# Kernel optimization log

Hardware: AMD Instinct MI355X
Metric: run time of the kernel (lower is better)

Reference implementation:

```python
import jax, jax.numpy as jnp
import numpy as np

N = 100000
E = 1600000
IN, HID, OUT = 128, 256, 128


def setup_inputs() -> dict:
    key = jax.random.key(0)
    ks = jax.random.split(key, 8)
    x = jax.random.normal(ks[0], (N, IN), dtype=jnp.float32)
    edge_index = jax.random.randint(ks[1], (2, E), 0, N, dtype=jnp.int64)
    # PyG SAGEConv params: lin_l (neighbor aggr, with bias), lin_r (root, no bias)
    def glorot(k, shape):
        fan_in = shape[1]
        return jax.random.normal(k, shape, dtype=jnp.float32) / jnp.sqrt(jnp.float32(fan_in))
    W1l = glorot(ks[2], (HID, IN)); b1 = jnp.zeros((HID,), jnp.float32)
    W1r = glorot(ks[3], (HID, IN))
    W2l = glorot(ks[4], (OUT, HID)); b2 = jnp.zeros((OUT,), jnp.float32)
    W2r = glorot(ks[5], (OUT, HID))
    return {"x": x, "edge_index": edge_index, "W1l": W1l, "b1": b1,
            "W1r": W1r, "W2l": W2l, "b2": b2, "W2r": W2r}


def sage_conv(x, row, col, Wl, b, Wr, n_nodes):
    # mean-aggregate neighbor features x[row] at target nodes col
    msg = x[row]                                               # [E, d]
    s = jax.ops.segment_sum(msg, col, num_segments=n_nodes)    # [N, d]
    deg = jax.ops.segment_sum(jnp.ones((row.shape[0], 1), x.dtype), col,
                              num_segments=n_nodes)            # [N, 1]
    mean = s / jnp.maximum(deg, 1.0)
    return mean @ Wl.T + b + x @ Wr.T


def reference(x, edge_index, W1l, b1, W1r, W2l, b2, W2r):
    row, col = edge_index[0], edge_index[1]
    h = sage_conv(x, row, col, W1l, b1, W1r, N)
    h = jax.nn.relu(h)
    # dropout is identity in eval mode
    out = sage_conv(h, row, col, W2l, b2, W2r, N)
    return out
```

## Files before the change

### kernel.cpp

```cpp
#include <hip/hip_runtime.h>
#include <hip/hip_bf16.h>
#include <hip/hip_fp16.h>

#define NN 100000
#define NE 1600000
#define NCHUNK ((NN + 127) / 128)
#define NPB 512
#define NB 256
#define CHUNK 8192
#define NCH ((NE + CHUNK - 1) / CHUNK)

typedef __attribute__((ext_vector_type(8))) short short8;
typedef __attribute__((ext_vector_type(4))) float float4v;
typedef __attribute__((ext_vector_type(2))) float float2v;

__device__ __forceinline__ unsigned short f2bf(float f) {
    unsigned int b = __float_as_uint(f);
    return (unsigned short)((b + 0x7fffu + ((b >> 16) & 1u)) >> 16);
}
__device__ __forceinline__ unsigned int pack_bf16(float lo, float hi) {
    return (unsigned int)f2bf(lo) | ((unsigned int)f2bf(hi) << 16);
}
__device__ __forceinline__ void addp8(float* a, uint2 u) {
    float2v f;
    f = __builtin_amdgcn_cvt_pk_f32_fp8(u.x, false); a[0] += f.x; a[1] += f.y;
    f = __builtin_amdgcn_cvt_pk_f32_fp8(u.x, true);  a[2] += f.x; a[3] += f.y;
    f = __builtin_amdgcn_cvt_pk_f32_fp8(u.y, false); a[4] += f.x; a[5] += f.y;
    f = __builtin_amdgcn_cvt_pk_f32_fp8(u.y, true);  a[6] += f.x; a[7] += f.y;
}
__device__ __forceinline__ unsigned char f2fp8(float v) {
    int r = __builtin_amdgcn_cvt_pk_fp8_f32(v, v, 0, false);
    return (unsigned char)(r & 0xff);
}
__device__ __forceinline__ unsigned short pack2fp8(float lo, float hi) {
    int r = __builtin_amdgcn_cvt_pk_fp8_f32(lo, hi, 0, false);
    return (unsigned short)(r & 0xffff);
}
__device__ __forceinline__ float h2f(unsigned short u) {
    return __half2float(__ushort_as_half(u));
}

__global__ void k_prep(const float* x, const float* W1l, const float* W1r,
                       const float* W2l, const float* W2r, const int* ei,
                       unsigned int* axb_u, unsigned short* xf8, unsigned short* wb1,
                       unsigned short* wb2, int* bcnt) {
    __shared__ int hh[NB];
    int b = blockIdx.x, t = threadIdx.x;
    if (b < 25000) {
        int tt = b * 256 + t;
        int node = tt >> 6, i = tt & 63;
        float2 v = ((const float2*)x)[tt];
        axb_u[(size_t)node * 128 + 64 + i] = pack_bf16(v.x, v.y);
        xf8[(size_t)node * 64 + i] = pack2fp8(v.x, v.y);
    } else if (b < 25128) {
        int i = (b - 25000) * 256 + t;
        int r1 = i >> 7, c1 = i & 127;
        wb1[r1 * 256 + c1]       = f2bf(W1l[i]);
        wb1[r1 * 256 + 128 + c1] = f2bf(W1r[i]);
        wb2[i]         = f2bf(W2l[i]);
        wb2[32768 + i] = f2bf(W2r[i]);
    } else {
        hh[t] = 0;
        __syncthreads();
        int e0 = (b - 25128) * 6250;
        for (int e = e0 + t; e < e0 + 6250; e += 256)
            atomicAdd(&hh[ei[NE + e] >> 9], 1);
        __syncthreads();
        if (hh[t]) atomicAdd(&bcnt[t], hh[t]);
    }
}

__global__ void k_bscan(const int* bcnt, int* boff, int* bcur) {
    __shared__ int s[NB];
    int t = threadIdx.x;
    int v = bcnt[t];
    s[t] = v;
    __syncthreads();
    for (int d = 1; d < NB; d <<= 1) {
        int val = (t >= d) ? s[t - d] : 0;
        __syncthreads();
        s[t] += val;
        __syncthreads();
    }
    boff[t + 1] = s[t];
    if (t == 0) boff[0] = 0;
    bcur[t] = s[t] - v;
}

__global__ __launch_bounds__(256) void k_bscatter(const int* ei, int* bcur, unsigned int* pairs) {
    __shared__ unsigned int buf[CHUNK];
    __shared__ int cnt[NB];
    __shared__ int lbase[NB];
    __shared__ int lcur[NB];
    __shared__ int gpos[NB];
    int t = threadIdx.x;
    int e0 = blockIdx.x * CHUNK;
    int nedge = NE - e0; if (nedge > CHUNK) nedge = CHUNK;
    cnt[t] = 0;
    __syncthreads();
    for (int i = t; i < nedge; i += 256)
        atomicAdd(&cnt[ei[NE + e0 + i] >> 9], 1);
    __syncthreads();
    int v = cnt[t];
    lcur[t] = v;
    __syncthreads();
    for (int d = 1; d < NB; d <<= 1) {
        int val = (t >= d) ? lcur[t - d] : 0;
        __syncthreads();
        lcur[t] += val;
        __syncthreads();
    }
    lbase[t] = lcur[t] - v;
    gpos[t] = atomicAdd(&bcur[t], v);
    __syncthreads();
    lcur[t] = lbase[t];
    __syncthreads();
    for (int i = t; i < nedge; i += 256) {
        int r = ei[e0 + i], c = ei[NE + e0 + i];
        int b = c >> 9;
        int p = atomicAdd(&lcur[b], 1);
        buf[p] = (unsigned)r | ((unsigned)(c & 511) << 17);
    }
    __syncthreads();
    int wv = t >> 6, lane = t & 63;
    for (int b = wv; b < NB; b += 4) {
        int n = cnt[b], lb = lbase[b], gp = gpos[b];
        for (int i = lane; i < n; i += 64)
            pairs[gp + i] = buf[lb + i];
    }
}

__global__ __launch_bounds__(256) void k_build(const unsigned int* pairs, const int* boff,
                                               int* off, int* deg, int* csr) {
    __shared__ int ldeg[NPB];
    __shared__ int lcur[NPB];
    __shared__ int sscan[256];
    int b = blockIdx.x;
    int nbase = b * NPB;
    if (nbase >= NN) return;
    int t = threadIdx.x;
    int base = boff[b], cntb = boff[b + 1] - base;
    ldeg[t] = 0; ldeg[t + 256] = 0;
    __syncthreads();
    for (int i = t; i < cntb; i += 256) {
        unsigned int pr = pairs[base + i];
        atomicAdd(&ldeg[pr >> 17], 1);
    }
    __syncthreads();
    int d0 = ldeg[2 * t], d1 = ldeg[2 * t + 1];
    int v = d0 + d1;
    sscan[t] = v;
    __syncthreads();
    for (int d = 1; d < 256; d <<= 1) {
        int val = (t >= d) ? sscan[t - d] : 0;
        __syncthreads();
        sscan[t] += val;
        __syncthreads();
    }
    int ex = sscan[t] - v;
    lcur[2 * t] = ex; lcur[2 * t + 1] = ex + d0;
    __syncthreads();
    int nloc = NN - nbase; if (nloc > NPB) nloc = NPB;
    for (int ln = t; ln < nloc; ln += 256) {
        off[nbase + ln] = base + lcur[ln];
        deg[nbase + ln] = ldeg[ln];
    }
    __syncthreads();
    for (int i = t; i < cntb; i += 256) {
        unsigned int pr = pairs[base + i];
        int p = atomicAdd(&lcur[pr >> 17], 1);
        csr[base + p] = (int)(pr & 0x1FFFFu);
    }
}

__global__ void k_agg1(const uint2* xf8, const int* off, const int* deg,
                       const int* csr, unsigned int* axb_w) {
    int wid = (blockIdx.x * 256 + threadIdx.x) >> 6;
    if (wid >= NN) return;
    int lane = threadIdx.x & 63;
    int sub = lane >> 4, l16 = lane & 15;
    int start = off[wid], d = deg[wid];
    const uint2* gp = xf8 + l16;
    float a[8] = {0.f, 0.f, 0.f, 0.f, 0.f, 0.f, 0.f, 0.f};
    int j = sub;
    for (; j + 4 < d; j += 8) {
        int n0 = csr[start + j];
        int n1 = csr[start + j + 4];
        uint2 u0 = gp[(size_t)n0 * 16];
        uint2 u1 = gp[(size_t)n1 * 16];
        addp8(a, u0); addp8(a, u1);
    }
    if (j < d) {
        int nb = csr[start + j];
        uint2 u = gp[(size_t)nb * 16];
        addp8(a, u);
    }
#pragma unroll
    for (int i = 0; i < 8; i++) {
        a[i] += __shfl_xor(a[i], 16, 64);
        a[i] += __shfl_xor(a[i], 32, 64);
    }
    if (sub == 0) {
        float inv = 1.0f / (float)(d > 0 ? d : 1);
        uint4 o;
        o.x = pack_bf16(a[0] * inv, a[1] * inv);
        o.y = pack_bf16(a[2] * inv, a[3] * inv);
        o.z = pack_bf16(a[4] * inv, a[5] * inv);
        o.w = pack_bf16(a[6] * inv, a[7] * inv);
        *(uint4*)(axb_w + (size_t)wid * 128 + (l16 << 2)) = o;
    }
}

__global__ void k_agg2(const uint2* g, const int* off, const int* deg,
                       const int* csr, const unsigned short* partial, float* out) {
    int wid = (blockIdx.x * 256 + threadIdx.x) >> 6;
    if (wid >= NN) return;
    int lane = threadIdx.x & 63;
    int sub = lane >> 4, l16 = lane & 15;
    int start = off[wid], d = deg[wid];
    const uint2* gp = g + l16;
    float a[8] = {0.f, 0.f, 0.f, 0.f, 0.f, 0.f, 0.f, 0.f};
    int j = sub;
    for (; j + 4 < d; j += 8) {
        int n0 = csr[start + j];
        int n1 = csr[start + j + 4];
        uint2 u0 = gp[(size_t)n0 * 16];
        uint2 u1 = gp[(size_t)n1 * 16];
        addp8(a, u0); addp8(a, u1);
    }
    if (j < d) {
        int nb = csr[start + j];
        uint2 u = gp[(size_t)nb * 16];
        addp8(a, u);
    }
#pragma unroll
    for (int i = 0; i < 8; i++) {
        a[i] += __shfl_xor(a[i], 16, 64);
        a[i] += __shfl_xor(a[i], 32, 64);
    }
    if (sub == 0) {
        float inv = 1.0f / (float)(d > 0 ? d : 1);
        uint4 pu = *(const uint4*)(partial + (size_t)wid * 128 + (l16 << 3));
        float4 c0, c1;
        c0.x = h2f(pu.x & 0xffff) + a[0] * inv; c0.y = h2f(pu.x >> 16) + a[1] * inv;
        c0.z = h2f(pu.y & 0xffff) + a[2] * inv; c0.w = h2f(pu.y >> 16) + a[3] * inv;
        c1.x = h2f(pu.z & 0xffff) + a[4] * inv; c1.y = h2f(pu.z >> 16) + a[5] * inv;
        c1.z = h2f(pu.w & 0xffff) + a[6] * inv; c1.w = h2f(pu.w >> 16) + a[7] * inv;
        float4* po = (float4*)(out + (size_t)wid * 128) + (l16 << 1);
        po[0] = c0; po[1] = c1;
    }
}

#define BROW 264
__global__ __launch_bounds__(256, 4) void k_gemm1(const unsigned short* A, const unsigned short* wb,
                                                  const float* b1, unsigned short* H) {
    __shared__ unsigned short Bs[64 * BROW];
    int t = threadIdx.x;
    int cg = blockIdx.x & 3, chunk = blockIdx.x >> 2;
    {
        const short8* src = (const short8*)(wb + (size_t)cg * 64 * 256);
        short8* dst = (short8*)Bs;
#pragma unroll
        for (int i = 0; i < 8; i++) {
            int gi = i * 256 + t;
            int r = gi >> 5, c = gi & 31;
            dst[r * 33 + c] = src[gi];
        }
    }
    __syncthreads();
    int wv = t >> 6, lane = t & 63;
    int mrow = lane & 15, quad = lane >> 4;
    int base = chunk * 128 + wv * 32;
    if (base >= NN) return;
    float bias[4];
#pragma unroll
    for (int ctl = 0; ctl < 4; ctl++) bias[ctl] = b1[cg * 64 + ctl * 16 + mrow];
    float4v acc[2][4];
#pragma unroll
    for (int h = 0; h < 2; h++)
#pragma unroll
        for (int ctl = 0; ctl < 4; ctl++) acc[h][ctl] = (float4v)(0.0f);
    const short8* a0p = (const short8*)(A + (size_t)(base + mrow) * 256);
    const short8* a1p = (const short8*)(A + (size_t)(base + 16 + mrow) * 256);
#pragma unroll
    for (int kk = 0; kk < 8; kk++) {
        short8 a0 = a0p[kk * 4 + quad];
        short8 a1 = a1p[kk * 4 + quad];
        int koff = kk * 32 + quad * 8;
#pragma unroll
        for (int ctl = 0; ctl < 4; ctl++) {
            short8 b = *(const short8*)(Bs + (ctl * 16 + mrow) * BROW + koff);
            acc[0][ctl] = __builtin_amdgcn_mfma_f32_16x16x32_bf16(a0, b, acc[0][ctl], 0, 0, 0);
            acc[1][ctl] = __builtin_amdgcn_mfma_f32_16x16x32_bf16(a1, b, acc[1][ctl], 0, 0, 0);
        }
    }
#pragma unroll
    for (int ctl = 0; ctl < 4; ctl++) {
        int col = cg * 64 + ctl * 16 + mrow;
#pragma unroll
        for (int h = 0; h < 2; h++)
#pragma unroll
            for (int r = 0; r < 4; r++) {
                int node = base + h * 16 + quad * 4 + r;
                float v = acc[h][ctl][r] + bias[ctl];
                H[(size_t)node * 256 + col] = f2bf(fmaxf(v, 0.f));
            }
    }
}

__global__ __launch_bounds__(256, 4) void k_gemm2(const unsigned short* A, const unsigned short* wb,
                                                  const float* b2, unsigned char* g,
                                                  unsigned short* partial) {
    __shared__ unsigned short Bs[64 * BROW];
    int t = threadIdx.x;
    int cg = blockIdx.x & 3, chunk = blockIdx.x >> 2;
    {
        const short8* src = (const short8*)(wb + (size_t)cg * 64 * 256);
        short8* dst = (short8*)Bs;
#pragma unroll
        for (int i = 0; i < 8; i++) {
            int gi = i * 256 + t;
            int r = gi >> 5, c = gi & 31;
            dst[r * 33 + c] = src[gi];
        }
    }
    __syncthreads();
    int wv = t >> 6, lane = t & 63;
    int mrow = lane & 15, quad = lane >> 4;
    int base = chunk * 128 + wv * 32;
    if (base >= NN) return;
    float bias[4];
#pragma unroll
    for (int ctl = 0; ctl < 4; ctl++)
        bias[ctl] = (cg >= 2) ? b2[cg * 64 + ctl * 16 + mrow - 128] : 0.f;
    float4v acc[2][4];
#pragma unroll
    for (int h = 0; h < 2; h++)
#pragma unroll
        for (int ctl = 0; ctl < 4; ctl++) acc[h][ctl] = (float4v)(0.0f);
    const short8* a0p = (const short8*)(A + (size_t)(base + mrow) * 256);
    const short8* a1p = (const short8*)(A + (size_t)(base + 16 + mrow) * 256);
#pragma unroll
    for (int kk = 0; kk < 8; kk++) {
        short8 a0 = a0p[kk * 4 + quad];
        short8 a1 = a1p[kk * 4 + quad];
        int koff = kk * 32 + quad * 8;
#pragma unroll
        for (int ctl = 0; ctl < 4; ctl++) {
            short8 b = *(const short8*)(Bs + (ctl * 16 + mrow) * BROW + koff);
            acc[0][ctl] = __builtin_amdgcn_mfma_f32_16x16x32_bf16(a0, b, acc[0][ctl], 0, 0, 0);
            acc[1][ctl] = __builtin_amdgcn_mfma_f32_16x16x32_bf16(a1, b, acc[1][ctl], 0, 0, 0);
        }
    }
    if (cg < 2) {
#pragma unroll
        for (int ctl = 0; ctl < 4; ctl++) {
            int col = cg * 64 + ctl * 16 + mrow;
#pragma unroll
            for (int h = 0; h < 2; h++)
#pragma unroll
                for (int r = 0; r < 4; r++) {
                    int node = base + h * 16 + quad * 4 + r;
                    g[(size_t)node * 128 + col] = f2fp8(acc[h][ctl][r]);
                }
        }
    } else {
#pragma unroll
        for (int ctl = 0; ctl < 4; ctl++) {
            int pcol = cg * 64 + ctl * 16 + mrow - 128;
#pragma unroll
            for (int h = 0; h < 2; h++)
#pragma unroll
                for (int r = 0; r < 4; r++) {
                    int node = base + h * 16 + quad * 4 + r;
                    __half hf = __float2half(acc[h][ctl][r] + bias[ctl]);
                    partial[(size_t)node * 128 + pcol] = __half_as_ushort(hf);
                }
        }
    }
}

extern "C" void kernel_launch(void* const* d_in, const int* in_sizes, int n_in,
                              void* d_out, int out_size, void* d_ws, size_t ws_size,
                              hipStream_t stream) {
    const float* x   = (const float*)d_in[0];
    const int*   ei  = (const int*)d_in[1];
    const float* W1l = (const float*)d_in[2];
    const float* b1  = (const float*)d_in[3];
    const float* W1r = (const float*)d_in[4];
    const float* W2l = (const float*)d_in[5];
    const float* b2  = (const float*)d_in[6];
    const float* W2r = (const float*)d_in[7];
    float* out = (float*)d_out;

    char* p = (char*)d_ws;
    unsigned int* axb = (unsigned int*)p; p += (size_t)NN * 256 * 2;
    unsigned short* h = (unsigned short*)p; p += (size_t)NN * 256 * 2;
    unsigned char* g  = (unsigned char*)p; p += (size_t)NN * 128;
    unsigned short* xf8 = (unsigned short*)p; p += (size_t)NN * 128;
    unsigned short* wb1 = (unsigned short*)p; p += 65536 * 2;
    unsigned short* wb2 = (unsigned short*)p; p += 65536 * 2;
    int* deg  = (int*)p; p += (size_t)NN * 4;
    int* off  = (int*)p; p += (size_t)NN * 4;
    int* csr  = (int*)p; p += (size_t)NE * 4;
    int* bcnt = (int*)p; p += NB * 4;
    int* boff = (int*)p; p += (NB + 1) * 4;
    int* bcur = (int*)p; p += NB * 4;
    if (ws_size < (size_t)(p - (char*)d_ws)) return;
    unsigned int* pairs = (unsigned int*)h;
    unsigned short* partial = (unsigned short*)axb;

    hipMemsetAsync(bcnt, 0, NB * 4, stream);
    k_prep<<<25384, 256, 0, stream>>>(x, W1l, W1r, W2l, W2r, ei, axb, xf8, wb1, wb2, bcnt);
    k_bscan<<<1, NB, 0, stream>>>(bcnt, boff, bcur);
    k_bscatter<<<NCH, 256, 0, stream>>>(ei, bcur, pairs);
    k_build<<<NB, 256, 0, stream>>>(pairs, boff, off, deg, csr);
    k_agg1<<<NN * 64 / 256, 256, 0, stream>>>((const uint2*)xf8, off, deg, csr, axb);
    k_gemm1<<<NCHUNK * 4, 256, 0, stream>>>((const unsigned short*)axb, wb1, b1, h);
    k_gemm2<<<NCHUNK * 4, 256, 0, stream>>>(h, wb2, b2, g, partial);
    k_agg2<<<25000, 256, 0, stream>>>((const uint2*)g, off, deg, csr, partial, out);
}
```

Before: 373.3 us.

## Make aggregation kernels persistent with software-pipelined index prefetch; regroup GEMM blocks

The two neighbor-aggregation kernels now use a persistent grid of 8192 waves. Each wave walks nodes with stride AGGW and prefetches the next node's offset, degree and first 16 CSR indices while it gathers the current node's features. This is meant to hide the dependent latency of off/deg to csr to feature loads, and it also unrolls the first 16 neighbor gathers. The GEMM kernels change their block-to-(chunk, column-group) mapping so that 8 consecutive blocks share the same weight column group, which may improve cache locality. The gain depends on whether fewer resident waves per node still give enough memory-level parallelism.

```diff
diff --git a/kernel.cpp b/kernel.cpp
--- a/kernel.cpp
+++ b/kernel.cpp
@@ -9,6 +9,7 @@
 #define NB 256
 #define CHUNK 8192
 #define NCH ((NE + CHUNK - 1) / CHUNK)
+#define AGGW 8192
 
 typedef __attribute__((ext_vector_type(8))) short short8;
 typedef __attribute__((ext_vector_type(4))) float float4v;
@@ -173,90 +174,147 @@
     }
 }
 
-__global__ void k_agg1(const uint2* xf8, const int* off, const int* deg,
-                       const int* csr, unsigned int* axb_w) {
-    int wid = (blockIdx.x * 256 + threadIdx.x) >> 6;
-    if (wid >= NN) return;
+__global__ __launch_bounds__(256) void k_agg1(const uint2* xf8, const int* off, const int* deg,
+                                              const int* csr, unsigned int* axb_w) {
+    int gw = (blockIdx.x * 256 + threadIdx.x) >> 6;
     int lane = threadIdx.x & 63;
     int sub = lane >> 4, l16 = lane & 15;
-    int start = off[wid], d = deg[wid];
     const uint2* gp = xf8 + l16;
-    float a[8] = {0.f, 0.f, 0.f, 0.f, 0.f, 0.f, 0.f, 0.f};
-    int j = sub;
-    for (; j + 4 < d; j += 8) {
-        int n0 = csr[start + j];
-        int n1 = csr[start + j + 4];
-        uint2 u0 = gp[(size_t)n0 * 16];
-        uint2 u1 = gp[(size_t)n1 * 16];
-        addp8(a, u0); addp8(a, u1);
-    }
-    if (j < d) {
-        int nb = csr[start + j];
-        uint2 u = gp[(size_t)nb * 16];
-        addp8(a, u);
-    }
-#pragma unroll
-    for (int i = 0; i < 8; i++) {
-        a[i] += __shfl_xor(a[i], 16, 64);
-        a[i] += __shfl_xor(a[i], 32, 64);
-    }
-    if (sub == 0) {
-        float inv = 1.0f / (float)(d > 0 ? d : 1);
-        uint4 o;
-        o.x = pack_bf16(a[0] * inv, a[1] * inv);
-        o.y = pack_bf16(a[2] * inv, a[3] * inv);
-        o.z = pack_bf16(a[4] * inv, a[5] * inv);
-        o.w = pack_bf16(a[6] * inv, a[7] * inv);
-        *(uint4*)(axb_w + (size_t)wid * 128 + (l16 << 2)) = o;
-    }
-}
-
-__global__ void k_agg2(const uint2* g, const int* off, const int* deg,
-                       const int* csr, const unsigned short* partial, float* out) {
-    int wid = (blockIdx.x * 256 + threadIdx.x) >> 6;
-    if (wid >= NN) return;
+    uint2 z; z.x = 0u; z.y = 0u;
+
+    int nA = gw;
+    int offA = off[nA], degA = deg[nA];
+    int nB = nA + AGGW;
+    int offB = 0, degB = 0;
+    if (nB < NN) { offB = off[nB]; degB = deg[nB]; }
+    int jA = sub;
+    int iA0 = csr[min(offA + jA,      NE - 1)];
+    int iA1 = csr[min(offA + jA + 4,  NE - 1)];
+    int iA2 = csr[min(offA + jA + 8,  NE - 1)];
+    int iA3 = csr[min(offA + jA + 12, NE - 1)];
+
+    while (true) {
+        uint2 u0 = (jA      < degA) ? gp[(size_t)iA0 * 16] : z;
+        uint2 u1 = (jA + 4  < degA) ? gp[(size_t)iA1 * 16] : z;
+        uint2 u2 = (jA + 8  < degA) ? gp[(size_t)iA2 * 16] : z;
+        uint2 u3 = (jA + 12 < degA) ? gp[(size_t)iA3 * 16] : z;
+        int jB = sub;
+        int iB0 = 0, iB1 = 0, iB2 = 0, iB3 = 0;
+        if (nB < NN) {
+            iB0 = csr[min(offB + jB,      NE - 1)];
+            iB1 = csr[min(offB + jB + 4,  NE - 1)];
+            iB2 = csr[min(offB + jB + 8,  NE - 1)];
+            iB3 = csr[min(offB + jB + 12, NE - 1)];
+        }
+        int nC = nB + AGGW;
+        int offC = 0, degC = 0;
+        if (nC < NN) { offC = off[nC]; degC = deg[nC]; }
+        float a[8] = {0.f, 0.f, 0.f, 0.f, 0.f, 0.f, 0.f, 0.f};
+        addp8(a, u0); addp8(a, u1); addp8(a, u2); addp8(a, u3);
+        for (int j = 16 + sub; j < degA; j += 4) {
+            int nb = csr[offA + j];
+            uint2 u = gp[(size_t)nb * 16];
+            addp8(a, u);
+        }
+#pragma unroll
+        for (int i = 0; i < 8; i++) {
+            a[i] += __shfl_xor(a[i], 16, 64);
+            a[i] += __shfl_xor(a[i], 32, 64);
+        }
+        if (sub == 0) {
+            float inv = 1.0f / (float)(degA > 0 ? degA : 1);
+            uint4 o;
+            o.x = pack_bf16(a[0] * inv, a[1] * inv);
+            o.y = pack_bf16(a[2] * inv, a[3] * inv);
+            o.z = pack_bf16(a[4] * inv, a[5] * inv);
+            o.w = pack_bf16(a[6] * inv, a[7] * inv);
+            *(uint4*)(axb_w + (size_t)nA * 128 + (l16 << 2)) = o;
+        }
+        nA = nB; offA = offB; degA = degB;
+        iA0 = iB0; iA1 = iB1; iA2 = iB2; iA3 = iB3; jA = jB;
+        nB = nC; offB = offC; degB = degC;
+        if (nA >= NN) break;
+    }
+}
+
+__global__ __launch_bounds__(256) void k_agg2(const uint2* g, const int* off, const int* deg,
+                                              const int* csr, const unsigned short* partial,
+                                              float* out) {
+    int gw = (blockIdx.x * 256 + threadIdx.x) >> 6;
     int lane = threadIdx.x & 63;
     int sub = lane >> 4, l16 = lane & 15;
-    int start = off[wid], d = deg[wid];
     const uint2* gp = g + l16;
-    float a[8] = {0.f, 0.f, 0.f, 0.f, 0.f, 0.f, 0.f, 0.f};
-    int j = sub;
-    for (; j + 4 < d; j += 8) {
-        int n0 = csr[start + j];
-        int n1 = csr[start + j + 4];
-        uint2 u0 = gp[(size_t)n0 * 16];
-        uint2 u1 = gp[(size_t)n1 * 16];
-        addp8(a, u0); addp8(a, u1);
-    }
-    if (j < d) {
-        int nb = csr[start + j];
-        uint2 u = gp[(size_t)nb * 16];
-        addp8(a, u);
-    }
-#pragma unroll
-    for (int i = 0; i < 8; i++) {
-        a[i] += __shfl_xor(a[i], 16, 64);
-        a[i] += __shfl_xor(a[i], 32, 64);
-    }
-    if (sub == 0) {
-        float inv = 1.0f / (float)(d > 0 ? d : 1);
-        uint4 pu = *(const uint4*)(partial + (size_t)wid * 128 + (l16 << 3));
-        float4 c0, c1;
-        c0.x = h2f(pu.x & 0xffff) + a[0] * inv; c0.y = h2f(pu.x >> 16) + a[1] * inv;
-        c0.z = h2f(pu.y & 0xffff) + a[2] * inv; c0.w = h2f(pu.y >> 16) + a[3] * inv;
-        c1.x = h2f(pu.z & 0xffff) + a[4] * inv; c1.y = h2f(pu.z >> 16) + a[5] * inv;
-        c1.z = h2f(pu.w & 0xffff) + a[6] * inv; c1.w = h2f(pu.w >> 16) + a[7] * inv;
-        float4* po = (float4*)(out + (size_t)wid * 128) + (l16 << 1);
-        po[0] = c0; po[1] = c1;
+    uint2 z; z.x = 0u; z.y = 0u;
+
+    int nA = gw;
+    int offA = off[nA], degA = deg[nA];
+    int nB = nA + AGGW;
+    int offB = 0, degB = 0;
+    if (nB < NN) { offB = off[nB]; degB = deg[nB]; }
+    int jA = sub;
+    int iA0 = csr[min(offA + jA,      NE - 1)];
+    int iA1 = csr[min(offA + jA + 4,  NE - 1)];
+    int iA2 = csr[min(offA + jA + 8,  NE - 1)];
+    int iA3 = csr[min(offA + jA + 12, NE - 1)];
+
+    while (true) {
+        uint2 u0 = (jA      < degA) ? gp[(size_t)iA0 * 16] : z;
+        uint2 u1 = (jA + 4  < degA) ? gp[(size_t)iA1 * 16] : z;
+        uint2 u2 = (jA + 8  < degA) ? gp[(size_t)iA2 * 16] : z;
+        uint2 u3 = (jA + 12 < degA) ? gp[(size_t)iA3 * 16] : z;
+        int jB = sub;
+        int iB0 = 0, iB1 = 0, iB2 = 0, iB3 = 0;
+        if (nB < NN) {
+            iB0 = csr[min(offB + jB,      NE - 1)];
+            iB1 = csr[min(offB + jB + 4,  NE - 1)];
+            iB2 = csr[min(offB + jB + 8,  NE - 1)];
+            iB3 = csr[min(offB + jB + 12, NE - 1)];
+        }
+        int nC = nB + AGGW;
+        int offC = 0, degC = 0;
+        if (nC < NN) { offC = off[nC]; degC = deg[nC]; }
+        uint4 pu;
+        if (sub == 0)
+            pu = *(const uint4*)(partial + (size_t)nA * 128 + (l16 << 3));
+        float a[8] = {0.f, 0.f, 0.f, 0.f, 0.f, 0.f, 0.f, 0.f};
+        addp8(a, u0); addp8(a, u1); addp8(a, u2); addp8(a, u3);
+        for (int j = 16 + sub; j < degA; j += 4) {
+            int nb = csr[offA + j];
+            uint2 u = gp[(size_t)nb * 16];
+            addp8(a, u);
+        }
+#pragma unroll
+        for (int i = 0; i < 8; i++) {
+            a[i] += __shfl_xor(a[i], 16, 64);
+            a[i] += __shfl_xor(a[i], 32, 64);
+        }
+        if (sub == 0) {
+            float inv = 1.0f / (float)(degA > 0 ? degA : 1);
+            float4 c0, c1;
+            c0.x = h2f(pu.x & 0xffff) + a[0] * inv; c0.y = h2f(pu.x >> 16) + a[1] * inv;
+            c0.z = h2f(pu.y & 0xffff) + a[2] * inv; c0.w = h2f(pu.y >> 16) + a[3] * inv;
+            c1.x = h2f(pu.z & 0xffff) + a[4] * inv; c1.y = h2f(pu.z >> 16) + a[5] * inv;
+            c1.z = h2f(pu.w & 0xffff) + a[6] * inv; c1.w = h2f(pu.w >> 16) + a[7] * inv;
+            float4* po = (float4*)(out + (size_t)nA * 128) + (l16 << 1);
+            po[0] = c0; po[1] = c1;
+        }
+        nA = nB; offA = offB; degA = degB;
+        iA0 = iB0; iA1 = iB1; iA2 = iB2; iA3 = iB3; jA = jB;
+        nB = nC; offB = offC; degB = degC;
+        if (nA >= NN) break;
     }
 }
 
 #define BROW 264
+#define GGRID (32 * ((NCHUNK + 7) / 8))
 __global__ __launch_bounds__(256, 4) void k_gemm1(const unsigned short* A, const unsigned short* wb,
                                                   const float* b1, unsigned short* H) {
     __shared__ unsigned short Bs[64 * BROW];
     int t = threadIdx.x;
-    int cg = blockIdx.x & 3, chunk = blockIdx.x >> 2;
+    int b = blockIdx.x;
+    int chunk = (b & 7) + ((b >> 5) << 3);
+    int cg = (b >> 3) & 3;
+    if (chunk >= NCHUNK) return;
     {
         const short8* src = (const short8*)(wb + (size_t)cg * 64 * 256);
         short8* dst = (short8*)Bs;
@@ -289,9 +347,9 @@
         int koff = kk * 32 + quad * 8;
 #pragma unroll
         for (int ctl = 0; ctl < 4; ctl++) {
-            short8 b = *(const short8*)(Bs + (ctl * 16 + mrow) * BROW + koff);
-            acc[0][ctl] = __builtin_amdgcn_mfma_f32_16x16x32_bf16(a0, b, acc[0][ctl], 0, 0, 0);
-            acc[1][ctl] = __builtin_amdgcn_mfma_f32_16x16x32_bf16(a1, b, acc[1][ctl], 0, 0, 0);
+            short8 bfr = *(const short8*)(Bs + (ctl * 16 + mrow) * BROW + koff);
+            acc[0][ctl] = __builtin_amdgcn_mfma_f32_16x16x32_bf16(a0, bfr, acc[0][ctl], 0, 0, 0);
+            acc[1][ctl] = __builtin_amdgcn_mfma_f32_16x16x32_bf16(a1, bfr, acc[1][ctl], 0, 0, 0);
         }
     }
 #pragma unroll
@@ -313,7 +371,10 @@
                                                   unsigned short* partial) {
     __shared__ unsigned short Bs[64 * BROW];
     int t = threadIdx.x;
-    int cg = blockIdx.x & 3, chunk = blockIdx.x >> 2;
+    int b = blockIdx.x;
+    int chunk = (b & 7) + ((b >> 5) << 3);
+    int cg = (b >> 3) & 3;
+    if (chunk >= NCHUNK) return;
     {
         const short8* src = (const short8*)(wb + (size_t)cg * 64 * 256);
         short8* dst = (short8*)Bs;
@@ -347,9 +408,9 @@
         int koff = kk * 32 + quad * 8;
 #pragma unroll
         for (int ctl = 0; ctl < 4; ctl++) {
-            short8 b = *(const short8*)(Bs + (ctl * 16 + mrow) * BROW + koff);
-            acc[0][ctl] = __builtin_amdgcn_mfma_f32_16x16x32_bf16(a0, b, acc[0][ctl], 0, 0, 0);
-            acc[1][ctl] = __builtin_amdgcn_mfma_f32_16x16x32_bf16(a1, b, acc[1][ctl], 0, 0, 0);
+            short8 bfr = *(const short8*)(Bs + (ctl * 16 + mrow) * BROW + koff);
+            acc[0][ctl] = __builtin_amdgcn_mfma_f32_16x16x32_bf16(a0, bfr, acc[0][ctl], 0, 0, 0);
+            acc[1][ctl] = __builtin_amdgcn_mfma_f32_16x16x32_bf16(a1, bfr, acc[1][ctl], 0, 0, 0);
         }
     }
     if (cg < 2) {
@@ -415,8 +476,8 @@
     k_bscan<<<1, NB, 0, stream>>>(bcnt, boff, bcur);
     k_bscatter<<<NCH, 256, 0, stream>>>(ei, bcur, pairs);
     k_build<<<NB, 256, 0, stream>>>(pairs, boff, off, deg, csr);
-    k_agg1<<<NN * 64 / 256, 256, 0, stream>>>((const uint2*)xf8, off, deg, csr, axb);
-    k_gemm1<<<NCHUNK * 4, 256, 0, stream>>>((const unsigned short*)axb, wb1, b1, h);
-    k_gemm2<<<NCHUNK * 4, 256, 0, stream>>>(h, wb2, b2, g, partial);
-    k_agg2<<<25000, 256, 0, stream>>>((const uint2*)g, off, deg, csr, partial, out);
-}
+    k_agg1<<<AGGW / 4, 256, 0, stream>>>((const uint2*)xf8, off, deg, csr, axb);
+    k_gemm1<<<GGRID, 256, 0, stream>>>((const unsigned short*)axb, wb1, b1, h);
+    k_gemm2<<<GGRID, 256, 0, stream>>>(h, wb2, b2, g, partial);
+    k_agg2<<<AGGW / 4, 256, 0, stream>>>((const uint2*)g, off, deg, csr, partial, out);
+}
```

Result: no change. 366.6 us (-1.8%).
